# Kernel optimization log

Hardware: AMD Instinct MI355X
Metric: run time of the kernel (lower is better)

The kernel has to match this reference:

```python
import jax, jax.numpy as jnp
import numpy as np

B, S_IN, T_OUT, H, L, V = 64, 512, 64, 1024, 2, 1024


def setup_inputs() -> dict:
    key = jax.random.key(0)
    ks = iter(jax.random.split(key, 64))
    def p(shape, scale=0.02):
        return (jax.random.normal(next(ks), shape, jnp.float32) * scale)
    d = {"x": jax.random.normal(next(ks), (B, 2, S_IN), jnp.float32)}
    d["emb"] = p((V, H))
    for l in range(L):
        i = 2 if l == 0 else H
        d[f"enc_Wih{l}"] = p((3 * H, i)); d[f"enc_Whh{l}"] = p((3 * H, H))
        d[f"enc_bih{l}"] = p((3 * H,));   d[f"enc_bhh{l}"] = p((3 * H,))
        d[f"dec_Wih{l}"] = p((H, H));     d[f"dec_Whh{l}"] = p((H, H))
        d[f"dec_bih{l}"] = p((H,));       d[f"dec_bhh{l}"] = p((H,))
    d["hq_W"] = p((H, H)); d["hq_b"] = p((H,))
    d["comb_W"] = p((H, 2 * H)); d["comb_b"] = p((H,))
    d["fc_W"] = p((V, H)); d["fc_b"] = p((V,))
    return d


def _gru_layer(x_seq, Wih, Whh, bih, bhh):
    # x_seq: [B,T,I] -> (outputs [B,T,H], h_T [B,H]). PyTorch GRU gate order r,z,n.
    xp = jnp.einsum('bti,gi->btg', x_seq, Wih) + bih  # [B,T,3H]
    h0 = jnp.zeros((x_seq.shape[0], Whh.shape[1]), x_seq.dtype)
    def step(h, xpt):
        hp = h @ Whh.T + bhh
        xr, xz, xn = jnp.split(xpt, 3, axis=-1)
        hr, hz, hn = jnp.split(hp, 3, axis=-1)
        r = jax.nn.sigmoid(xr + hr)
        z = jax.nn.sigmoid(xz + hz)
        n = jnp.tanh(xn + r * hn)
        h = (1.0 - z) * n + z * h
        return h, h
    hT, ys = jax.lax.scan(step, h0, jnp.swapaxes(xp, 0, 1))
    return jnp.swapaxes(ys, 0, 1), hT


def _forward(x, emb,
             enc_Wih0, enc_Whh0, enc_bih0, enc_bhh0,
             enc_Wih1, enc_Whh1, enc_bih1, enc_bhh1,
             dec_Wih0, dec_Whh0, dec_bih0, dec_bhh0,
             dec_Wih1, dec_Whh1, dec_bih1, dec_bhh1,
             hq_W, hq_b, comb_W, comb_b, fc_W, fc_b):
    enc_params = [(enc_Wih0, enc_Whh0, enc_bih0, enc_bhh0),
                  (enc_Wih1, enc_Whh1, enc_bih1, enc_bhh1)]
    dec_params = [(dec_Wih0, dec_Whh0, dec_bih0, dec_bhh0),
                  (dec_Wih1, dec_Whh1, dec_bih1, dec_bhh1)]
    # ---- encoder: GRU over x permuted to [B, S_in, 2] ----
    seq = jnp.transpose(x, (0, 2, 1)).astype(jnp.float32)
    h_enc = []
    for (Wih, Whh, bih, bhh) in enc_params:
        seq, hT = _gru_layer(seq, Wih, Whh, bih, bhh)
        h_enc.append(hT)
    enc_outs = seq                      # [B, S_in, H]
    hidden0 = jnp.stack(h_enc, axis=0)  # [L, B, H]

    tok0 = jnp.zeros((B,), jnp.int32)
    def dec_step(carry, _):
        tok, hid = carry
        inp = emb[tok]                  # [B, H]
        new_h = []
        for l, (Wih, Whh, bih, bhh) in enumerate(dec_params):
            h = jnp.tanh(inp @ Wih.T + bih + hid[l] @ Whh.T + bhh)
            new_h.append(h)
            inp = h
        hid = jnp.stack(new_h, axis=0)
        q = inp @ hq_W.T + hq_b                          # [B, H]
        scores = jnp.einsum('bsh,bh->bs', enc_outs, q)   # [B, S_in]
        aw = jax.nn.softmax(scores, axis=1)
        att = jnp.einsum('bs,bsh->bh', aw, enc_outs)     # [B, H]
        logits = jnp.concatenate([inp, att], axis=-1) @ comb_W.T + comb_b
        logits = logits @ fc_W.T + fc_b                  # [B, V]
        tok = jnp.argmax(logits, axis=-1).astype(jnp.int32)
        return (tok, hid), (logits, aw)
    (_, hidden), (logits_t, aw_t) = jax.lax.scan(dec_step, (tok0, hidden0), None, length=T_OUT)
    vec_out = jnp.swapaxes(logits_t, 0, 1)   # [B, T_out, V]
    attn = aw_t[-1][:, None, :]              # [B, 1, S_in] (last step, as in source)
    return vec_out, hidden, attn


def reference(x, emb,
              enc_Wih0, enc_Whh0, enc_bih0, enc_bhh0,
              enc_Wih1, enc_Whh1, enc_bih1, enc_bhh1,
              dec_Wih0, dec_Whh0, dec_bih0, dec_bhh0,
              dec_Wih1, dec_Whh1, dec_bih1, dec_bhh1,
              hq_W, hq_b, comb_W, comb_b, fc_W, fc_b):
    return _forward(x, emb,
                    enc_Wih0, enc_Whh0, enc_bih0, enc_bhh0,
                    enc_Wih1, enc_Whh1, enc_bih1, enc_bhh1,
                    dec_Wih0, dec_Whh0, dec_bih0, dec_bhh0,
                    dec_Wih1, dec_Whh1, dec_bih1, dec_bhh1,
                    hq_W, hq_b, comb_W, comb_b, fc_W, fc_b)
```

## Files before the change

kernel.cpp:

```cpp
#include <hip/hip_runtime.h>
#include <stdint.h>


#define BB 64
#define SS 512
#define TT 64
#define HH 1024
#define VV 1024
#define BH 65536
#define SH 524288
#define OFF_HID  4194304
#define OFF_ATTN 4325376

typedef _Float16 half8  __attribute__((ext_vector_type(8)));
typedef float    floatx4 __attribute__((ext_vector_type(4)));

struct P {
  const float *x, *emb;
  const float *eWih0, *eWhh0, *ebih0, *ebhh0;
  const float *dWih0, *dWhh0, *dbih0, *dbhh0;
  const float *eWih1, *eWhh1, *ebih1, *ebhh1;
  const float *dWih1, *dWhh1, *dbih1, *dbhh1;
  const float *hqW, *hqb, *combW, *combb, *fcW, *fcb;
  uint32_t* enc_i;
  _Float16 *W0h,*W0l;
  _Float16 *W1h,*W1l;
  _Float16 *embh,*embl,*T0h,*T0l;
  _Float16 *wih0dh,*wih0dl,*wih1dh,*wih1dl,*whh0dh,*whh0dl,*whh1dh,*whh1dl;
  _Float16 *hqh,*hql,*combh,*combl,*fch,*fcl;
  _Float16 *h0h,*h0l,*h1h,*h1l;
  _Float16 *dh0h,*dh0l,*dh1h,*dh1l;
  _Float16 *cath,*catl;
  _Float16 *ch,*cl;
  float *u0,*u1,*w1x,*q;
  unsigned long long* amax;
  float* dout;
};

struct GSet { const _Float16 *Wh, *Wl, *Ah, *Al; const float *bias; float *out; };

__device__ __forceinline__ void splitf(float x, _Float16& hi, _Float16& lo){
  _Float16 h = (_Float16)x; hi = h;
  lo = (_Float16)((x - (float)h) * 2048.0f);
}
__device__ __forceinline__ float reconf(_Float16 hi, _Float16 lo){
  return fmaf((float)lo, 1.0f/2048.0f, (float)hi);
}
__device__ __forceinline__ float recon_u32(uint32_t w){
  float hi = (float)__builtin_bit_cast(_Float16, (unsigned short)(w & 0xffffu));
  float lo = (float)__builtin_bit_cast(_Float16, (unsigned short)(w >> 16));
  return fmaf(lo, 1.0f/2048.0f, hi);
}
__device__ __forceinline__ uint32_t pack_pair(float x){
  _Float16 hi, lo; splitf(x, hi, lo);
  return (uint32_t)__builtin_bit_cast(unsigned short, hi)
       | ((uint32_t)__builtin_bit_cast(unsigned short, lo) << 16);
}
__device__ __forceinline__ unsigned ordf(float f){
  unsigned u = __float_as_uint(f);
  return (u & 0x80000000u) ? ~u : (u | 0x80000000u);
}

template<int NT, int KH, bool SPLIT>
__device__ __forceinline__ void gemm_core(
    const _Float16* __restrict__ Ah0, const _Float16* __restrict__ Al0,
    const _Float16* __restrict__ Ah1, const _Float16* __restrict__ Al1,
    int sA,
    const _Float16* __restrict__ Wh, const _Float16* __restrict__ Wl,
    int nrows, _Float16* ldsW, float* accOut)
{
  const int tid = threadIdx.x, lane = tid & 63, wave = tid >> 6;
  const int mA = (wave<<4) + (lane & 15);
  const int kb = ((lane>>4) << 3);
  const int wstride = KH << 10;
  floatx4 aH[NT], aM1[NT], aM2[NT];
  int ne[NT];
  const _Float16* bh_base[NT];
  const _Float16* bl_base[NT];
  #pragma unroll
  for (int nt=0; nt<NT; ++nt){
    int nn = (lane & 15) + (nt<<4);
    ne[nt] = nn < nrows ? nn : nrows - 1;
    bh_base[nt] = ldsW + ne[nt]*1032 + kb;
    aH[nt]  = floatx4{0.f,0.f,0.f,0.f};
    aM1[nt] = floatx4{0.f,0.f,0.f,0.f};
    aM2[nt] = floatx4{0.f,0.f,0.f,0.f};
  }
  #pragma unroll
  for (int kh=0; kh<KH; ++kh){
    __syncthreads();
    const int iters = (nrows*128 + 255) >> 8;
    for (int it=0; it<iters; ++it){
      int idx = tid + (it<<8);
      int row = idx >> 7, col = (idx & 127) << 3;
      if (row < nrows)
        *(half8*)(ldsW + row*1032 + col) =
            *(const half8*)(Wh + row*wstride + (kh<<10) + col);
    }
    __syncthreads();
    const _Float16* ah_p = ((KH==2 && kh==1) ? Ah1 : Ah0) + mA*sA + kb;
    const _Float16* al_p = ((KH==2 && kh==1) ? Al1 : Al0) + mA*sA + kb;
    #pragma unroll
    for (int nt=0; nt<NT; ++nt) bl_base[nt] = Wl + ne[nt]*wstride + (kh<<10) + kb;
    #pragma unroll 4
    for (int ks=0; ks<32; ++ks){
      half8 ah = *(const half8*)(ah_p + (ks<<5));
      half8 al = *(const half8*)(al_p + (ks<<5));
      #pragma unroll
      for (int nt=0; nt<NT; ++nt){
        half8 bh = *(const half8*)(bh_base[nt] + (ks<<5));
        half8 bl = *(const half8*)(bl_base[nt] + (ks<<5));
        aH[nt]  = __builtin_amdgcn_mfma_f32_16x16x32_f16(ah, bh, aH[nt],  0,0,0);
        aM1[nt] = __builtin_amdgcn_mfma_f32_16x16x32_f16(ah, bl, aM1[nt], 0,0,0);
        aM2[nt] = __builtin_amdgcn_mfma_f32_16x16x32_f16(al, bh, aM2[nt], 0,0,0);
      }
    }
    if (SPLIT){
      #pragma unroll
      for (int nt=0; nt<NT; ++nt){
        #pragma unroll
        for (int r=0;r<4;++r)
          accOut[(kh*NT + nt)*4 + r] = aH[nt][r] + (aM1[nt][r] + aM2[nt][r]) * (1.f/2048.f);
        aH[nt]  = floatx4{0.f,0.f,0.f,0.f};
        aM1[nt] = floatx4{0.f,0.f,0.f,0.f};
        aM2[nt] = floatx4{0.f,0.f,0.f,0.f};
      }
    }
  }
  if (!SPLIT){
    #pragma unroll
    for (int nt=0; nt<NT; ++nt)
      #pragma unroll
      for (int r=0;r<4;++r)
        accOut[nt*4 + r] = aH[nt][r] + (aM1[nt][r] + aM2[nt][r]) * (1.f/2048.f);
  }
}

__global__ __launch_bounds__(256) void k_split(const float* __restrict__ src,
                                               _Float16* dh, _Float16* dl, int n){
  for (int i = blockIdx.x*256 + threadIdx.x; i < n; i += gridDim.x*256){
    _Float16 hi,lo; splitf(src[i],hi,lo); dh[i]=hi; dl[i]=lo;
  }
}

__global__ __launch_bounds__(256) void k_rw0(P p){
  const int n = 256*12*1024;
  for (int i = blockIdx.x*256 + threadIdx.x; i < n; i += gridDim.x*256){
    int k = i & 1023; int rest = i >> 10; int rr = rest % 12; int blk = rest / 12;
    int grow = (rr>>2)*1024 + (blk<<2) + (rr&3);
    _Float16 hi,lo; splitf(p.eWhh0[grow*1024 + k],hi,lo);
    p.W0h[i]=hi; p.W0l[i]=lo;
  }
}
__global__ __launch_bounds__(256) void k_rw1(P p){
  const int n = 256*12*2048;
  for (int i = blockIdx.x*256 + threadIdx.x; i < n; i += gridDim.x*256){
    int k = i & 2047; int rest = i >> 11; int rr = rest % 12; int blk = rest / 12;
    int grow = (rr>>2)*1024 + (blk<<2) + (rr&3);
    float v = (k < 1024) ? p.eWhh1[grow*1024 + k] : p.eWih1[grow*1024 + (k-1024)];
    _Float16 hi,lo; splitf(v,hi,lo);
    p.W1h[i]=hi; p.W1l[i]=lo;
  }
}
__global__ __launch_bounds__(256) void k_zero(P p){
  int i = blockIdx.x*256 + threadIdx.x;
  p.h1h[i] = (_Float16)0.f; p.h1l[i] = (_Float16)0.f;
  p.h0h[BH + i] = (_Float16)0.f; p.h0l[BH + i] = (_Float16)0.f;
}
__global__ __launch_bounds__(256) void k_t0(P p){
  __shared__ _Float16 ldsW[16*1032];
  const int ns = blockIdx.x & 63, mc = blockIdx.x >> 6;
  float acc[4];
  gemm_core<1,1,false>(p.embh + mc*65536, p.embl + mc*65536, nullptr, nullptr, 1024,
                       p.wih0dh + ns*16*1024, p.wih0dl + ns*16*1024, 16, ldsW, acc);
  const int lane = threadIdx.x & 63, wave = threadIdx.x >> 6;
  const int n = lane & 15, col = (ns<<4) + n;
  const float bv = p.dbih0[col];
  #pragma unroll
  for (int r=0;r<4;++r){
    int v = mc*64 + (wave<<4) + ((lane>>4)<<2) + r;
    _Float16 hi,lo; splitf(acc[r] + bv, hi, lo);
    p.T0h[v*1024 + col] = hi; p.T0l[v*1024 + col] = lo;
  }
}

__global__ __launch_bounds__(256,2) void k_enc(P p, int e){
  __shared__ _Float16 ldsW[24768];
  __shared__ float ldsG[2*12*68];
  __shared__ float ldsC[12*4];
  const int tid = threadIdx.x, lane = tid & 63, wave = tid >> 6;
  const bool is0 = blockIdx.x < 256;
  if (is0 && e >= 512) return;
  if (!is0 && e < 1) return;
  const int blk = is0 ? (int)blockIdx.x : (int)blockIdx.x - 256;
  const int j0 = blk << 2;

  if (is0){
    const _Float16* gh = p.W0h + blk*12*1024;
    const _Float16* gl = p.W0l + blk*12*1024;
    _Float16* Wl = ldsW + 12*1032;
    for (int it = tid; it < 12*128; it += 256){
      int row = it >> 7, col = (it & 127) << 3;
      *(half8*)(ldsW + row*1032 + col) = *(const half8*)(gh + row*1024 + col);
      *(half8*)(Wl   + row*1032 + col) = *(const half8*)(gl + row*1024 + col);
    }
  } else {
    const _Float16* gh = p.W1h + blk*12*2048;
    for (int it = tid; it < 12*256; it += 256){
      int row = it >> 8, col = (it & 255) << 3;
      *(half8*)(ldsW + row*2056 + col) = *(const half8*)(gh + row*2048 + col);
    }
  }
  if (tid < 12){
    int grow = (tid>>2)*1024 + j0 + (tid & 3);
    if (is0){
      ldsC[tid*4+0] = p.eWih0[grow*2+0];
      ldsC[tid*4+1] = p.eWih0[grow*2+1];
      ldsC[tid*4+2] = p.ebih0[grow];
      ldsC[tid*4+3] = p.ebhh0[grow];
    } else {
      ldsC[tid*4+0] = p.ebih1[grow];
      ldsC[tid*4+1] = p.ebhh1[grow];
    }
  }
  __syncthreads();

  const int cur = e & 1, prv = cur ^ 1;
  const int mA = (wave<<4) + (lane & 15);
  const int kb = ((lane>>4) << 3);
  const int nn = lane & 15;
  const int ne = nn < 12 ? nn : 11;
  const int b_ep = tid & 63, c_ep = tid >> 6;
  const int col_ep = j0 + c_ep;

  if (is0){
    floatx4 aH{0.f,0.f,0.f,0.f}, aM1{0.f,0.f,0.f,0.f}, aM2{0.f,0.f,0.f,0.f};
    const _Float16* ah_p = p.h0h + prv*BH + mA*1024 + kb;
    const _Float16* al_p = p.h0l + prv*BH + mA*1024 + kb;
    const _Float16* bh_p = ldsW + ne*1032 + kb;
    const _Float16* bl_p = ldsW + 12*1032 + ne*1032 + kb;
    #pragma unroll 4
    for (int ks=0; ks<32; ++ks){
      half8 ah = *(const half8*)(ah_p + (ks<<5));
      half8 al = *(const half8*)(al_p + (ks<<5));
      half8 bh = *(const half8*)(bh_p + (ks<<5));
      half8 bl = *(const half8*)(bl_p + (ks<<5));
      aH  = __builtin_amdgcn_mfma_f32_16x16x32_f16(ah, bh, aH,  0,0,0);
      aM1 = __builtin_amdgcn_mfma_f32_16x16x32_f16(ah, bl, aM1, 0,0,0);
      aM2 = __builtin_amdgcn_mfma_f32_16x16x32_f16(al, bh, aM2, 0,0,0);
    }
    if (nn < 12){
      #pragma unroll
      for (int r=0;r<4;++r)
        ldsG[nn*68 + (wave<<4)+((lane>>4)<<2)+r] =
            aH[r] + (aM1[r] + aM2[r]) * (1.f/2048.f);
    }
    __syncthreads();
    {
      const int b = b_ep, c = c_ep, col = col_ep;
      float hr = ldsG[c*68+b]     + ldsC[c*4+3];
      float hz = ldsG[(4+c)*68+b] + ldsC[(4+c)*4+3];
      float hn = ldsG[(8+c)*68+b] + ldsC[(8+c)*4+3];
      float x0 = p.x[b*1024 + e], x1 = p.x[b*1024 + 512 + e];
      float xr = fmaf(x0, ldsC[c*4+0],     fmaf(x1, ldsC[c*4+1],     ldsC[c*4+2]));
      float xz = fmaf(x0, ldsC[(4+c)*4+0], fmaf(x1, ldsC[(4+c)*4+1], ldsC[(4+c)*4+2]));
      float xn = fmaf(x0, ldsC[(8+c)*4+0], fmaf(x1, ldsC[(8+c)*4+1], ldsC[(8+c)*4+2]));
      float rg = 1.0f/(1.0f + expf(-(xr+hr)));
      float zg = 1.0f/(1.0f + expf(-(xz+hz)));
      float ng = tanhf(xn + rg*hn);
      float hold = reconf(p.h0h[prv*BH + b*1024 + col], p.h0l[prv*BH + b*1024 + col]);
      float hnew = (1.0f - zg)*ng + zg*hold;
      _Float16 hi,lo; splitf(hnew,hi,lo);
      p.h0h[cur*BH + b*1024 + col] = hi;
      p.h0l[cur*BH + b*1024 + col] = lo;
    }
  } else {
    #pragma unroll
    for (int kh=0; kh<2; ++kh){
      floatx4 aH{0.f,0.f,0.f,0.f}, aM1{0.f,0.f,0.f,0.f}, aM2{0.f,0.f,0.f,0.f};
      const _Float16* ah_p = (kh ? p.h0h : p.h1h) + prv*BH + mA*1024 + kb;
      const _Float16* al_p = (kh ? p.h0l : p.h1l) + prv*BH + mA*1024 + kb;
      const _Float16* bh_p = ldsW + ne*2056 + (kh<<10) + kb;
      const _Float16* bl_p = p.W1l + blk*12*2048 + ne*2048 + (kh<<10) + kb;
      #pragma unroll 4
      for (int ks=0; ks<32; ++ks){
        half8 ah = *(const half8*)(ah_p + (ks<<5));
        half8 al = *(const half8*)(al_p + (ks<<5));
        half8 bh = *(const half8*)(bh_p + (ks<<5));
        half8 bl = *(const half8*)(bl_p + (ks<<5));
        aH  = __builtin_amdgcn_mfma_f32_16x16x32_f16(ah, bh, aH,  0,0,0);
        aM1 = __builtin_amdgcn_mfma_f32_16x16x32_f16(ah, bl, aM1, 0,0,0);
        aM2 = __builtin_amdgcn_mfma_f32_16x16x32_f16(al, bh, aM2, 0,0,0);
      }
      if (nn < 12){
        #pragma unroll
        for (int r=0;r<4;++r)
          ldsG[(kh*12+nn)*68 + (wave<<4)+((lane>>4)<<2)+r] =
              aH[r] + (aM1[r] + aM2[r]) * (1.f/2048.f);
      }
    }
    __syncthreads();
    {
      const int b = b_ep, c = c_ep, col = col_ep;
      const int t = e - 1;
      float hr = ldsG[c*68+b]        + ldsC[c*4+1];
      float hz = ldsG[(4+c)*68+b]    + ldsC[(4+c)*4+1];
      float hn = ldsG[(8+c)*68+b]    + ldsC[(8+c)*4+1];
      float xr = ldsG[(12+c)*68+b]   + ldsC[c*4+0];
      float xz = ldsG[(12+4+c)*68+b] + ldsC[(4+c)*4+0];
      float xn = ldsG[(12+8+c)*68+b] + ldsC[(8+c)*4+0];
      float rg = 1.0f/(1.0f + expf(-(xr+hr)));
      float zg = 1.0f/(1.0f + expf(-(xz+hz)));
      float ng = tanhf(xn + rg*hn);
      float hold = reconf(p.h1h[prv*BH + b*1024 + col], p.h1l[prv*BH + b*1024 + col]);
      float hnew = (1.0f - zg)*ng + zg*hold;
      _Float16 hi,lo; splitf(hnew,hi,lo);
      p.h1h[cur*BH + b*1024 + col] = hi;
      p.h1l[cur*BH + b*1024 + col] = lo;
      p.enc_i[b*SH + t*1024 + col] = pack_pair(hnew);
    }
  }
}

__global__ __launch_bounds__(256) void k_dgemm2(GSet a, GSet b){
  const int tid = threadIdx.x, lane = tid & 63, wave = tid >> 6;
  const GSet g = blockIdx.x < 128 ? a : b;
  const int blk = blockIdx.x & 127;
  __shared__ _Float16 ldsW[8*1032];
  float acc[4];
  gemm_core<1,1,false>(g.Ah, g.Al, nullptr, nullptr, 1024,
                       g.Wh + blk*8*1024, g.Wl + blk*8*1024, 8, ldsW, acc);
  int n = lane & 15;
  if (n < 8){
    int col = (blk<<3) + n;
    float bv = g.bias[col];
    #pragma unroll
    for (int r=0;r<4;++r){
      int m = (wave<<4)+((lane>>4)<<2)+r;
      g.out[m*1024 + col] = acc[r] + bv;
    }
  }
}

__global__ __launch_bounds__(256) void k_dgemm2h1(P p, GSet a, GSet b){
  const int tid = threadIdx.x, lane = tid & 63, wave = tid >> 6;
  const bool isa = blockIdx.x < 128;
  const GSet g = isa ? a : b;
  const int blk = blockIdx.x & 127;
  __shared__ _Float16 ldsW[8*1032];
  float acc[4];
  gemm_core<1,1,false>(g.Ah, g.Al, nullptr, nullptr, 1024,
                       g.Wh + blk*8*1024, g.Wl + blk*8*1024, 8, ldsW, acc);
  int n = lane & 15;
  if (n < 8){
    int col = (blk<<3) + n;
    float bv = g.bias[col];
    if (isa){
      #pragma unroll
      for (int r=0;r<4;++r){
        int m = (wave<<4)+((lane>>4)<<2)+r;
        float val = tanhf((acc[r] + bv) + p.u1[m*1024 + col]);
        _Float16 hi,lo; splitf(val,hi,lo);
        p.dh1h[m*1024+col]=hi; p.dh1l[m*1024+col]=lo;
        p.cath[m*2048+col]=hi; p.catl[m*2048+col]=lo;
      }
    } else {
      #pragma unroll
      for (int r=0;r<4;++r){
        int m = (wave<<4)+((lane>>4)<<2)+r;
        g.out[m*1024 + col] = acc[r] + bv;
      }
    }
  }
}

__global__ __launch_bounds__(256) void k_dec0(P p, int t){
  const int tid = threadIdx.x, b = blockIdx.x;
  __shared__ unsigned long long red[256];
  unsigned long long v = 0;
  if (t > 0 && tid < 128) v = p.amax[b*128 + tid];
  red[tid] = v; __syncthreads();
  for (int off=128; off>=1; off>>=1){
    if (tid < off){ unsigned long long o = red[tid+off]; if (o > red[tid]) red[tid] = o; }
    __syncthreads();
  }
  const int tokb = (t > 0) ? (1023 - (int)(red[0] & 0xffffffffULL)) : 0;
  #pragma unroll
  for (int i=0;i<4;++i){
    int h = tid + (i<<8);
    float val = tanhf(reconf(p.T0h[tokb*1024+h], p.T0l[tokb*1024+h]) + p.u0[b*1024+h]);
    _Float16 hi,lo; splitf(val,hi,lo);
    p.dh0h[b*1024+h]=hi; p.dh0l[b*1024+h]=lo;
  }
}
__global__ __launch_bounds__(512) void k_flash8(P p, int t){
  const int tid = threadIdx.x, lane = tid & 63, wave = tid >> 6;
  const int b = blockIdx.x;
  const bool last = (t == 63);
  float qv[16];
  #pragma unroll
  for (int i=0;i<16;++i) qv[i] = p.q[b*1024 + (i<<6) + lane];
  float ov[16];
  #pragma unroll
  for (int i=0;i<16;++i) ov[i] = 0.f;
  __shared__ float ldsO[8][1024];
  __shared__ float ldsM[8], ldsL2[8];
  __shared__ float ldsS[512];
  float mrun = -3.0e38f, lrun = 0.f;
  for (int si=0; si<64; ++si){
    int s = (wave<<6) + si;
    const uint32_t* ep = p.enc_i + b*SH + s*1024 + lane;
    float ef[16]; float partial = 0.f;
    #pragma unroll
    for (int i=0;i<16;++i){
      ef[i] = recon_u32(ep[i<<6]);
      partial = fmaf(ef[i], qv[i], partial);
    }
    #pragma unroll
    for (int off=32; off; off>>=1) partial += __shfl_xor(partial, off, 64);
    if (last && lane == 0) ldsS[s] = partial;
    float mnew = fmaxf(mrun, partial);
    float fac = __expf(mrun - mnew);
    float w   = __expf(partial - mnew);
    lrun = fmaf(lrun, fac, w);
    #pragma unroll
    for (int i=0;i<16;++i) ov[i] = fmaf(ov[i], fac, w*ef[i]);
    mrun = mnew;
  }
  #pragma unroll
  for (int i=0;i<16;++i) ldsO[wave][(i<<6)+lane] = ov[i];
  if (lane == 0){ ldsM[wave] = mrun; ldsL2[wave] = lrun; }
  __syncthreads();
  float M0 = fmaxf(fmaxf(ldsM[0],ldsM[1]), fmaxf(ldsM[2],ldsM[3]));
  float g0 = __expf(ldsM[0]-M0), g1 = __expf(ldsM[1]-M0),
        g2 = __expf(ldsM[2]-M0), g3 = __expf(ldsM[3]-M0);
  float lH0 = g0*ldsL2[0] + g1*ldsL2[1] + g2*ldsL2[2] + g3*ldsL2[3];
  float M1 = fmaxf(fmaxf(ldsM[4],ldsM[5]), fmaxf(ldsM[6],ldsM[7]));
  float g4 = __expf(ldsM[4]-M1), g5 = __expf(ldsM[5]-M1),
        g6 = __expf(ldsM[6]-M1), g7 = __expf(ldsM[7]-M1);
  float lH1 = g4*ldsL2[4] + g5*ldsL2[5] + g6*ldsL2[6] + g7*ldsL2[7];
  float M = fmaxf(M0,M1);
  float F0 = expf(M0-M), F1 = expf(M1-M);
  float invL = 1.0f/(F0*lH0 + F1*lH1);
  #pragma unroll
  for (int i=0;i<2;++i){
    int h = tid + (i<<9);
    float a0 = g0*ldsO[0][h] + g1*ldsO[1][h] + g2*ldsO[2][h] + g3*ldsO[3][h];
    float a1 = g4*ldsO[4][h] + g5*ldsO[5][h] + g6*ldsO[6][h] + g7*ldsO[7][h];
    float o = (F0*a0 + F1*a1) * invL;
    _Float16 hi,lo; splitf(o,hi,lo);
    p.cath[b*2048 + 1024 + h] = hi; p.catl[b*2048 + 1024 + h] = lo;
  }
  if (last){
    int s = tid;
    p.dout[OFF_ATTN + b*512 + s] = expf(ldsS[s] - M) * invL;
  }
}
__global__ __launch_bounds__(256) void k_comb(P p){
  const int tid = threadIdx.x, lane = tid & 63, wave = tid >> 6;
  const int blk = blockIdx.x;
  __shared__ _Float16 ldsW[8*1032];
  float acc[4];
  gemm_core<1,2,false>(p.cath, p.catl, p.cath + 1024, p.catl + 1024, 2048,
                       p.combh + blk*8*2048, p.combl + blk*8*2048, 8, ldsW, acc);
  int n = lane & 15;
  if (n < 8){
    int col = (blk<<3) + n;
    float bv = p.combb[col];
    #pragma unroll
    for (int r=0;r<4;++r){
      int m = (wave<<4)+((lane>>4)<<2)+r;
      _Float16 hi,lo; splitf(acc[r] + bv, hi, lo);
      p.ch[m*1024 + col] = hi; p.cl[m*1024 + col] = lo;
    }
  }
}
__global__ __launch_bounds__(256) void k_fc(P p, int t){
  const int tid = threadIdx.x, lane = tid & 63, wave = tid >> 6;
  const int blk = blockIdx.x;
  __shared__ _Float16 ldsW[8*1032];
  __shared__ float ldsL[8][68];
  float acc[4];
  gemm_core<1,1,false>(p.ch, p.cl, nullptr, nullptr, 1024,
                       p.fch + blk*8*1024, p.fcl + blk*8*1024, 8, ldsW, acc);
  int n = lane & 15;
  if (n < 8){
    int col = (blk<<3) + n;
    float bv = p.fcb[col];
    #pragma unroll
    for (int r=0;r<4;++r){
      int m = (wave<<4)+((lane>>4)<<2)+r;
      float val = acc[r] + bv;
      p.dout[m*65536 + t*1024 + col] = val;
      ldsL[n][m] = val;
    }
  }
  __syncthreads();
  if (tid < 64){
    int b = tid; float best = -3.0e38f; int bi = 0;
    #pragma unroll
    for (int jj=0; jj<8; ++jj){
      float v = ldsL[jj][b];
      if (v > best){ best = v; bi = jj; }
    }
    unsigned long long pk = ((unsigned long long)ordf(best) << 32)
                          | (unsigned)(1023 - ((blk<<3) + bi));
    p.amax[b*128 + blk] = pk;
  }
}
__global__ __launch_bounds__(256) void k_hidden(P p){
  int idx = blockIdx.x*256 + threadIdx.x;
  int i = idx & 65535;
  float v = (idx >> 16) ? reconf(p.dh1h[i], p.dh1l[i]) : reconf(p.dh0h[i], p.dh0l[i]);
  p.dout[OFF_HID + idx] = v;
}

extern "C" void kernel_launch(void* const* d_in, const int* in_sizes, int n_in,
                              void* d_out, int out_size, void* d_ws, size_t ws_size,
                              hipStream_t stream)
{
  (void)in_sizes; (void)n_in; (void)out_size;
  P p;
  p.x     = (const float*)d_in[0];  p.emb   = (const float*)d_in[1];
  p.eWih0 = (const float*)d_in[2];  p.eWhh0 = (const float*)d_in[3];
  p.ebih0 = (const float*)d_in[4];  p.ebhh0 = (const float*)d_in[5];
  p.dWih0 = (const float*)d_in[6];  p.dWhh0 = (const float*)d_in[7];
  p.dbih0 = (const float*)d_in[8];  p.dbhh0 = (const float*)d_in[9];
  p.eWih1 = (const float*)d_in[10]; p.eWhh1 = (const float*)d_in[11];
  p.ebih1 = (const float*)d_in[12]; p.ebhh1 = (const float*)d_in[13];
  p.dWih1 = (const float*)d_in[14]; p.dWhh1 = (const float*)d_in[15];
  p.dbih1 = (const float*)d_in[16]; p.dbhh1 = (const float*)d_in[17];
  p.hqW   = (const float*)d_in[18]; p.hqb   = (const float*)d_in[19];
  p.combW = (const float*)d_in[20]; p.combb = (const float*)d_in[21];
  p.fcW   = (const float*)d_in[22]; p.fcb   = (const float*)d_in[23];
  p.dout  = (float*)d_out;

  char* base = (char*)d_ws; size_t off = 0;
  auto alloc = [&](size_t bytes)->char*{
    char* r = base + off; off = (off + bytes + 255) & ~(size_t)255; return r;
  };
  p.enc_i = (uint32_t*)alloc(33554432ULL*4);
  p.W0h = (_Float16*)alloc(3145728ULL*2);  p.W0l = (_Float16*)alloc(3145728ULL*2);
  p.W1h = (_Float16*)alloc(6291456ULL*2);  p.W1l = (_Float16*)alloc(6291456ULL*2);
  p.embh = (_Float16*)alloc(1048576ULL*2); p.embl = (_Float16*)alloc(1048576ULL*2);
  p.T0h  = (_Float16*)alloc(1048576ULL*2); p.T0l  = (_Float16*)alloc(1048576ULL*2);
  p.wih0dh=(_Float16*)alloc(1048576ULL*2); p.wih0dl=(_Float16*)alloc(1048576ULL*2);
  p.wih1dh=(_Float16*)alloc(1048576ULL*2); p.wih1dl=(_Float16*)alloc(1048576ULL*2);
  p.whh0dh=(_Float16*)alloc(1048576ULL*2); p.whh0dl=(_Float16*)alloc(1048576ULL*2);
  p.whh1dh=(_Float16*)alloc(1048576ULL*2); p.whh1dl=(_Float16*)alloc(1048576ULL*2);
  p.hqh  = (_Float16*)alloc(1048576ULL*2); p.hql  = (_Float16*)alloc(1048576ULL*2);
  p.combh= (_Float16*)alloc(2097152ULL*2); p.combl= (_Float16*)alloc(2097152ULL*2);
  p.fch  = (_Float16*)alloc(1048576ULL*2); p.fcl  = (_Float16*)alloc(1048576ULL*2);
  p.h0h  = (_Float16*)alloc(131072ULL*2);  p.h0l  = (_Float16*)alloc(131072ULL*2);
  p.h1h  = (_Float16*)alloc(131072ULL*2);  p.h1l  = (_Float16*)alloc(131072ULL*2);
  p.dh0h = (_Float16*)alloc(65536ULL*2);   p.dh0l = (_Float16*)alloc(65536ULL*2);
  p.dh1h = (_Float16*)alloc(65536ULL*2);   p.dh1l = (_Float16*)alloc(65536ULL*2);
  p.cath = (_Float16*)alloc(131072ULL*2);  p.catl = (_Float16*)alloc(131072ULL*2);
  p.ch   = (_Float16*)alloc(65536ULL*2);   p.cl   = (_Float16*)alloc(65536ULL*2);
  p.u0   = (float*)alloc(65536ULL*4);      p.u1   = (float*)alloc(65536ULL*4);
  p.w1x  = (float*)alloc(65536ULL*4);      p.q    = (float*)alloc(65536ULL*4);
  p.amax    = (unsigned long long*)alloc(8192ULL*8);
  if (off > ws_size) return;

  k_split<<<2048,256,0,stream>>>(p.emb,   p.embh,   p.embl,   1048576);
  k_split<<<2048,256,0,stream>>>(p.dWih0, p.wih0dh, p.wih0dl, 1048576);
  k_split<<<2048,256,0,stream>>>(p.dWih1, p.wih1dh, p.wih1dl, 1048576);
  k_split<<<2048,256,0,stream>>>(p.dWhh0, p.whh0dh, p.whh0dl, 1048576);
  k_split<<<2048,256,0,stream>>>(p.dWhh1, p.whh1dh, p.whh1dl, 1048576);
  k_split<<<2048,256,0,stream>>>(p.hqW,   p.hqh,    p.hql,    1048576);
  k_split<<<2048,256,0,stream>>>(p.combW, p.combh,  p.combl,  2097152);
  k_split<<<2048,256,0,stream>>>(p.fcW,   p.fch,    p.fcl,    1048576);
  k_rw0<<<4096,256,0,stream>>>(p);
  k_rw1<<<4096,256,0,stream>>>(p);
  k_zero<<<256,256,0,stream>>>(p);
  k_t0<<<1024,256,0,stream>>>(p);

  for (int e=0; e<=512; ++e) k_enc<<<512,256,0,stream>>>(p, e);

  {
    GSet a{p.whh0dh, p.whh0dl, p.h0h + BH, p.h0l + BH, p.dbhh0, p.u0};
    GSet b{p.whh1dh, p.whh1dl, p.h1h,      p.h1l,      p.dbhh1, p.u1};
    k_dgemm2<<<256,256,0,stream>>>(a, b);
  }
  GSet sK1a{p.wih1dh, p.wih1dl, p.dh0h, p.dh0l, p.dbih1, p.w1x};
  GSet sK1b{p.whh0dh, p.whh0dl, p.dh0h, p.dh0l, p.dbhh0, p.u0};
  GSet sK3a{p.hqh,    p.hql,    p.dh1h, p.dh1l, p.hqb,   p.q};
  GSet sK3b{p.whh1dh, p.whh1dl, p.dh1h, p.dh1l, p.dbhh1, p.u1};

  for (int t=0; t<64; ++t){
    k_dec0<<<64,256,0,stream>>>(p, t);
    k_dgemm2h1<<<256,256,0,stream>>>(p, sK1a, sK1b);
    k_dgemm2<<<256,256,0,stream>>>(sK3a, sK3b);
    k_flash8<<<64,512,0,stream>>>(p, t);
    k_comb<<<128,256,0,stream>>>(p);
    k_fc<<<128,256,0,stream>>>(p, t);
  }
  k_hidden<<<512,256,0,stream>>>(p);
}
```

Baseline: 28.68 ms.

## Split encoder layer-1 work across 512 blocks and keep low-half weights in LDS

The encoder layer-1 GRU step is now spread over 512 blocks of 2 hidden columns each instead of 256 blocks of 4, so the grid grows to 768 blocks. The weight reorder kernel is changed to match the 6-row-per-block layout. The low-precision half of the split weights is now staged in LDS next to the high half, instead of being read from global memory inside the MFMA loop. This adds parallelism and removes global weight traffic on the serial encoder critical path, but half of each MFMA tile's N columns go unused and only 128 threads do epilogue work.

```diff
diff --git a/kernel.cpp b/kernel.cpp
--- a/kernel.cpp
+++ b/kernel.cpp
@@ -153,10 +153,10 @@
   }
 }
 __global__ __launch_bounds__(256) void k_rw1(P p){
-  const int n = 256*12*2048;
+  const int n = 512*6*2048;
   for (int i = blockIdx.x*256 + threadIdx.x; i < n; i += gridDim.x*256){
-    int k = i & 2047; int rest = i >> 11; int rr = rest % 12; int blk = rest / 12;
-    int grow = (rr>>2)*1024 + (blk<<2) + (rr&3);
+    int k = i & 2047; int rest = i >> 11; int rr = rest % 6; int blk = rest / 6;
+    int grow = (rr>>1)*1024 + (blk<<1) + (rr&1);
     float v = (k < 1024) ? p.eWhh1[grow*1024 + k] : p.eWih1[grow*1024 + (k-1024)];
     _Float16 hi,lo; splitf(v,hi,lo);
     p.W1h[i]=hi; p.W1l[i]=lo;
@@ -193,9 +193,9 @@
   if (is0 && e >= 512) return;
   if (!is0 && e < 1) return;
   const int blk = is0 ? (int)blockIdx.x : (int)blockIdx.x - 256;
-  const int j0 = blk << 2;
 
   if (is0){
+    const int j0 = blk << 2;
     const _Float16* gh = p.W0h + blk*12*1024;
     const _Float16* gl = p.W0l + blk*12*1024;
     _Float16* Wl = ldsW + 12*1032;
@@ -204,36 +204,21 @@
       *(half8*)(ldsW + row*1032 + col) = *(const half8*)(gh + row*1024 + col);
       *(half8*)(Wl   + row*1032 + col) = *(const half8*)(gl + row*1024 + col);
     }
-  } else {
-    const _Float16* gh = p.W1h + blk*12*2048;
-    for (int it = tid; it < 12*256; it += 256){
-      int row = it >> 8, col = (it & 255) << 3;
-      *(half8*)(ldsW + row*2056 + col) = *(const half8*)(gh + row*2048 + col);
-    }
-  }
-  if (tid < 12){
-    int grow = (tid>>2)*1024 + j0 + (tid & 3);
-    if (is0){
+    if (tid < 12){
+      int grow = (tid>>2)*1024 + j0 + (tid & 3);
       ldsC[tid*4+0] = p.eWih0[grow*2+0];
       ldsC[tid*4+1] = p.eWih0[grow*2+1];
       ldsC[tid*4+2] = p.ebih0[grow];
       ldsC[tid*4+3] = p.ebhh0[grow];
-    } else {
-      ldsC[tid*4+0] = p.ebih1[grow];
-      ldsC[tid*4+1] = p.ebhh1[grow];
-    }
-  }
-  __syncthreads();
-
-  const int cur = e & 1, prv = cur ^ 1;
-  const int mA = (wave<<4) + (lane & 15);
-  const int kb = ((lane>>4) << 3);
-  const int nn = lane & 15;
-  const int ne = nn < 12 ? nn : 11;
-  const int b_ep = tid & 63, c_ep = tid >> 6;
-  const int col_ep = j0 + c_ep;
-
-  if (is0){
+    }
+    __syncthreads();
+
+    const int cur = e & 1, prv = cur ^ 1;
+    const int mA = (wave<<4) + (lane & 15);
+    const int kb = ((lane>>4) << 3);
+    const int nn = lane & 15;
+    const int ne = nn < 12 ? nn : 11;
+
     floatx4 aH{0.f,0.f,0.f,0.f}, aM1{0.f,0.f,0.f,0.f}, aM2{0.f,0.f,0.f,0.f};
     const _Float16* ah_p = p.h0h + prv*BH + mA*1024 + kb;
     const _Float16* al_p = p.h0l + prv*BH + mA*1024 + kb;
@@ -257,7 +242,8 @@
     }
     __syncthreads();
     {
-      const int b = b_ep, c = c_ep, col = col_ep;
+      const int b = tid & 63, c = tid >> 6;
+      const int col = j0 + c;
       float hr = ldsG[c*68+b]     + ldsC[c*4+3];
       float hz = ldsG[(4+c)*68+b] + ldsC[(4+c)*4+3];
       float hn = ldsG[(8+c)*68+b] + ldsC[(8+c)*4+3];
@@ -275,13 +261,35 @@
       p.h0l[cur*BH + b*1024 + col] = lo;
     }
   } else {
+    const int j0 = blk << 1;
+    const _Float16* gh = p.W1h + blk*6*2048;
+    const _Float16* gl = p.W1l + blk*6*2048;
+    _Float16* Wl = ldsW + 6*2056;
+    for (int it = tid; it < 6*256; it += 256){
+      int row = it >> 8, col = (it & 255) << 3;
+      *(half8*)(ldsW + row*2056 + col) = *(const half8*)(gh + row*2048 + col);
+      *(half8*)(Wl   + row*2056 + col) = *(const half8*)(gl + row*2048 + col);
+    }
+    if (tid < 6){
+      int grow = (tid>>1)*1024 + j0 + (tid & 1);
+      ldsC[tid*4+0] = p.ebih1[grow];
+      ldsC[tid*4+1] = p.ebhh1[grow];
+    }
+    __syncthreads();
+
+    const int cur = e & 1, prv = cur ^ 1;
+    const int mA = (wave<<4) + (lane & 15);
+    const int kb = ((lane>>4) << 3);
+    const int nn = lane & 15;
+    const int ne = nn < 6 ? nn : 5;
+
     #pragma unroll
     for (int kh=0; kh<2; ++kh){
       floatx4 aH{0.f,0.f,0.f,0.f}, aM1{0.f,0.f,0.f,0.f}, aM2{0.f,0.f,0.f,0.f};
       const _Float16* ah_p = (kh ? p.h0h : p.h1h) + prv*BH + mA*1024 + kb;
       const _Float16* al_p = (kh ? p.h0l : p.h1l) + prv*BH + mA*1024 + kb;
       const _Float16* bh_p = ldsW + ne*2056 + (kh<<10) + kb;
-      const _Float16* bl_p = p.W1l + blk*12*2048 + ne*2048 + (kh<<10) + kb;
+      const _Float16* bl_p = ldsW + 6*2056 + ne*2056 + (kh<<10) + kb;
       #pragma unroll 4
       for (int ks=0; ks<32; ++ks){
         half8 ah = *(const half8*)(ah_p + (ks<<5));
@@ -292,23 +300,24 @@
         aM1 = __builtin_amdgcn_mfma_f32_16x16x32_f16(ah, bl, aM1, 0,0,0);
         aM2 = __builtin_amdgcn_mfma_f32_16x16x32_f16(al, bh, aM2, 0,0,0);
       }
-      if (nn < 12){
+      if (nn < 6){
         #pragma unroll
         for (int r=0;r<4;++r)
-          ldsG[(kh*12+nn)*68 + (wave<<4)+((lane>>4)<<2)+r] =
+          ldsG[(kh*6+nn)*68 + (wave<<4)+((lane>>4)<<2)+r] =
               aH[r] + (aM1[r] + aM2[r]) * (1.f/2048.f);
       }
     }
     __syncthreads();
-    {
-      const int b = b_ep, c = c_ep, col = col_ep;
+    if (tid < 128){
+      const int b = tid & 63, c = tid >> 6;
+      const int col = j0 + c;
       const int t = e - 1;
-      float hr = ldsG[c*68+b]        + ldsC[c*4+1];
-      float hz = ldsG[(4+c)*68+b]    + ldsC[(4+c)*4+1];
-      float hn = ldsG[(8+c)*68+b]    + ldsC[(8+c)*4+1];
-      float xr = ldsG[(12+c)*68+b]   + ldsC[c*4+0];
-      float xz = ldsG[(12+4+c)*68+b] + ldsC[(4+c)*4+0];
-      float xn = ldsG[(12+8+c)*68+b] + ldsC[(8+c)*4+0];
+      float hr = ldsG[(0+c)*68+b]   + ldsC[c*4+1];
+      float hz = ldsG[(2+c)*68+b]   + ldsC[(2+c)*4+1];
+      float hn = ldsG[(4+c)*68+b]   + ldsC[(4+c)*4+1];
+      float xr = ldsG[(6+c)*68+b]   + ldsC[c*4+0];
+      float xz = ldsG[(6+2+c)*68+b] + ldsC[(2+c)*4+0];
+      float xn = ldsG[(6+4+c)*68+b] + ldsC[(4+c)*4+0];
       float rg = 1.0f/(1.0f + expf(-(xr+hr)));
       float zg = 1.0f/(1.0f + expf(-(xz+hz)));
       float ng = tanhf(xn + rg*hn);
@@ -575,7 +584,7 @@
   k_zero<<<256,256,0,stream>>>(p);
   k_t0<<<1024,256,0,stream>>>(p);
 
-  for (int e=0; e<=512; ++e) k_enc<<<512,256,0,stream>>>(p, e);
+  for (int e=0; e<=512; ++e) k_enc<<<768,256,0,stream>>>(p, e);
 
   {
     GSet a{p.whh0dh, p.whh0dl, p.h0h + BH, p.h0l + BH, p.dbhh0, p.u0};
```

Measured after the change: 32.17 ms. +12.1%, slower.
